# Optimization experiments

Hardware: AMD Instinct MI355X
Metric: run time of the kernel (lower is better)

The kernel has to match this reference:

```python
import jax, jax.numpy as jnp
import numpy as np

N = 100000
D = 512


def setup_inputs() -> dict:
    key = jax.random.key(0)
    k1, k2 = jax.random.split(key)
    features = jax.random.normal(k1, (N, D), dtype=jnp.float32)
    attn_w = jax.random.normal(k2, (D,), dtype=jnp.float32)
    attn_b = jnp.zeros((1,), dtype=jnp.float32)
    return {"features": features, "attn_w": attn_w, "attn_b": attn_b, "k": 4}


def reference(features, attn_w, attn_b, k):
    # features: [N, D]; sliding-window (half-width k, truncated at edges) mean
    n = features.shape[0]
    zero = jnp.zeros((1, features.shape[1]), dtype=features.dtype)
    cs = jnp.concatenate([zero, jnp.cumsum(features, axis=0)], axis=0)  # [N+1, D]
    i = jnp.arange(n)
    lo = jnp.maximum(i - k, 0)          # inclusive window start
    hi = jnp.minimum(i + k, n - 1)      # inclusive window end
    win_sum = cs[hi + 1] - cs[lo]       # [N, D]
    count = (hi - lo + 1).astype(features.dtype)[:, None]
    agg = win_sum / count               # [N, D] windowed means
    scores = agg @ attn_w + attn_b[0]   # [N]
    w = jax.nn.softmax(scores, axis=0)  # [N]
    bag = w @ agg                       # [D]
    return bag, w
```

## Files before the change

### kernel.cpp

```cpp
#include <hip/hip_runtime.h>
#include <math.h>

#define D 512
#define NB_P 1000

__global__ void k_dot(const float* __restrict__ f, const float* __restrict__ w,
                      float* __restrict__ dot, int n) {
    int wave = threadIdx.x >> 6;
    int lane = threadIdx.x & 63;
    int row  = blockIdx.x * 4 + wave;
    if (row >= n) return;
    const float4* fr = (const float4*)(f + (size_t)row * D);
    const float4* wr = (const float4*)w;
    float4 a0 = fr[lane],      b0 = wr[lane];
    float4 a1 = fr[lane + 64], b1 = wr[lane + 64];
    float s = a0.x*b0.x + a0.y*b0.y + a0.z*b0.z + a0.w*b0.w
            + a1.x*b1.x + a1.y*b1.y + a1.z*b1.z + a1.w*b1.w;
    #pragma unroll
    for (int off = 32; off; off >>= 1) s += __shfl_down(s, off);
    if (lane == 0) dot[row] = s;
}

__global__ void k_scores(const float* __restrict__ dot, const float* __restrict__ bptr,
                         const int* __restrict__ kptr, float* __restrict__ scores,
                         float* __restrict__ pmax, float* __restrict__ psum, int n) {
    int i = blockIdx.x * 256 + threadIdx.x;
    int k = *kptr;
    float val = -INFINITY;
    if (i < n) {
        int lo = max(i - k, 0), hi = min(i + k, n - 1);
        float s = 0.f;
        for (int j = lo; j <= hi; ++j) s += dot[j];
        val = s / (float)(hi - lo + 1) + bptr[0];
        scores[i] = val;
    }
    __shared__ float sm[4];
    __shared__ float bmax;
    int lane = threadIdx.x & 63, wid = threadIdx.x >> 6;
    float m = val;
    #pragma unroll
    for (int off = 32; off; off >>= 1) m = fmaxf(m, __shfl_down(m, off));
    if (lane == 0) sm[wid] = m;
    __syncthreads();
    if (threadIdx.x == 0)
        bmax = fmaxf(fmaxf(sm[0], sm[1]), fmaxf(sm[2], sm[3]));
    __syncthreads();
    float mb = bmax;
    float e = (i < n) ? __expf(val - mb) : 0.f;
    #pragma unroll
    for (int off = 32; off; off >>= 1) e += __shfl_down(e, off);
    __syncthreads();
    if (lane == 0) sm[wid] = e;
    __syncthreads();
    if (threadIdx.x == 0) {
        pmax[blockIdx.x] = mb;
        psum[blockIdx.x] = sm[0] + sm[1] + sm[2] + sm[3];
    }
}

__global__ void k_wu(const float* __restrict__ scores, const float* __restrict__ pmax,
                     const float* __restrict__ psum, int nb1,
                     const int* __restrict__ kptr, float* __restrict__ w_out,
                     float* __restrict__ u, int n) {
    __shared__ float sm[4];
    __shared__ float gshared[2];
    int lane = threadIdx.x & 63, wid = threadIdx.x >> 6;

    float m = -INFINITY;
    for (int idx = threadIdx.x; idx < nb1; idx += 256) m = fmaxf(m, pmax[idx]);
    #pragma unroll
    for (int off = 32; off; off >>= 1) m = fmaxf(m, __shfl_down(m, off));
    if (lane == 0) sm[wid] = m;
    __syncthreads();
    if (threadIdx.x == 0)
        gshared[0] = fmaxf(fmaxf(sm[0], sm[1]), fmaxf(sm[2], sm[3]));
    __syncthreads();
    float gmax = gshared[0];

    float s = 0.f;
    for (int idx = threadIdx.x; idx < nb1; idx += 256)
        s += psum[idx] * __expf(pmax[idx] - gmax);
    #pragma unroll
    for (int off = 32; off; off >>= 1) s += __shfl_down(s, off);
    __syncthreads();
    if (lane == 0) sm[wid] = s;
    __syncthreads();
    if (threadIdx.x == 0)
        gshared[1] = 1.f / (sm[0] + sm[1] + sm[2] + sm[3]);
    __syncthreads();
    float inv = gshared[1];

    int j = blockIdx.x * 256 + threadIdx.x;
    if (j >= n) return;
    int k = *kptr;
    float ej = __expf(scores[j] - gmax);
    w_out[j] = ej * inv;
    int lo = max(j - k, 0), hi = min(j + k, n - 1);
    float acc = 0.f;
    for (int i = lo; i <= hi; ++i) {
        int li = max(i - k, 0), hh = min(i + k, n - 1);
        float e = __expf(scores[i] - gmax);
        acc += e * __builtin_amdgcn_rcpf((float)(hh - li + 1));
    }
    u[j] = acc * inv;
}

__global__ void k_pbag(const float* __restrict__ f, const float* __restrict__ u,
                       float* __restrict__ partial, int n, int chunk) {
    int t = threadIdx.x;
    int j0 = blockIdx.x * chunk;
    int j1 = min(j0 + chunk, n);
    float4 acc0 = make_float4(0.f,0.f,0.f,0.f);
    float4 acc1 = make_float4(0.f,0.f,0.f,0.f);
    float4 acc2 = make_float4(0.f,0.f,0.f,0.f);
    float4 acc3 = make_float4(0.f,0.f,0.f,0.f);
    int j = j0;
    for (; j + 4 <= j1; j += 4) {
        float u0 = u[j], u1 = u[j+1], u2 = u[j+2], u3 = u[j+3];
        float4 v0 = ((const float4*)(f + (size_t)(j  ) * D))[t];
        float4 v1 = ((const float4*)(f + (size_t)(j+1) * D))[t];
        float4 v2 = ((const float4*)(f + (size_t)(j+2) * D))[t];
        float4 v3 = ((const float4*)(f + (size_t)(j+3) * D))[t];
        acc0.x += u0*v0.x; acc0.y += u0*v0.y; acc0.z += u0*v0.z; acc0.w += u0*v0.w;
        acc1.x += u1*v1.x; acc1.y += u1*v1.y; acc1.z += u1*v1.z; acc1.w += u1*v1.w;
        acc2.x += u2*v2.x; acc2.y += u2*v2.y; acc2.z += u2*v2.z; acc2.w += u2*v2.w;
        acc3.x += u3*v3.x; acc3.y += u3*v3.y; acc3.z += u3*v3.z; acc3.w += u3*v3.w;
    }
    for (; j < j1; ++j) {
        float uj = u[j];
        float4 v = ((const float4*)(f + (size_t)j * D))[t];
        acc0.x += uj*v.x; acc0.y += uj*v.y; acc0.z += uj*v.z; acc0.w += uj*v.w;
    }
    float4 a;
    a.x = (acc0.x + acc1.x) + (acc2.x + acc3.x);
    a.y = (acc0.y + acc1.y) + (acc2.y + acc3.y);
    a.z = (acc0.z + acc1.z) + (acc2.z + acc3.z);
    a.w = (acc0.w + acc1.w) + (acc2.w + acc3.w);
    ((float4*)(partial + (size_t)blockIdx.x * D))[t] = a;
}

__global__ void k_rbag(const float* __restrict__ partial, float* __restrict__ bag, int nb) {
    int c = blockIdx.x * 16 + (threadIdx.x & 15);
    int r = threadIdx.x >> 4;
    float acc = 0.f;
    for (int b = r; b < nb; b += 16) acc += partial[(size_t)b * D + c];
    __shared__ float sm[256];
    sm[threadIdx.x] = acc;
    __syncthreads();
    if (threadIdx.x < 16) {
        float s = 0.f;
        #pragma unroll
        for (int q = 0; q < 16; ++q) s += sm[q * 16 + threadIdx.x];
        bag[blockIdx.x * 16 + threadIdx.x] = s;
    }
}

extern "C" void kernel_launch(void* const* d_in, const int* in_sizes, int n_in,
                              void* d_out, int out_size, void* d_ws, size_t ws_size,
                              hipStream_t stream) {
    const float* f  = (const float*)d_in[0];
    const float* aw = (const float*)d_in[1];
    const float* ab = (const float*)d_in[2];
    const int*   kp = (const int*)d_in[3];
    int n = in_sizes[0] / D;

    float* bag   = (float*)d_out;
    float* w_out = (float*)d_out + D;

    int nb2 = (n + 255) / 256;

    float* wsf     = (float*)d_ws;
    float* dot     = wsf;
    float* scores  = wsf + n;
    float* u       = wsf + 2 * (size_t)n;
    float* pmax    = wsf + 3 * (size_t)n;
    float* psum    = pmax + nb2;
    size_t poff    = ((3 * (size_t)n + 2 * (size_t)nb2) + 31) & ~(size_t)31;
    float* partial = wsf + poff;

    int chunk = (n + NB_P - 1) / NB_P;

    k_dot   <<<(n + 3) / 4, 256, 0, stream>>>(f, aw, dot, n);
    k_scores<<<nb2, 256, 0, stream>>>(dot, ab, kp, scores, pmax, psum, n);
    k_wu    <<<nb2, 256, 0, stream>>>(scores, pmax, psum, nb2, kp, w_out, u, n);
    k_pbag  <<<NB_P, 128, 0, stream>>>(f, u, partial, n, chunk);
    k_rbag  <<<32, 256, 0, stream>>>(partial, bag, NB_P);
}
```

Baseline: 90.74 us.

## Drop softmax max pass and fold normalization into final reduction kernel

```diff
diff --git a/kernel.cpp b/kernel.cpp
--- a/kernel.cpp
+++ b/kernel.cpp
@@ -21,88 +21,37 @@
     if (lane == 0) dot[row] = s;
 }
 
-__global__ void k_scores(const float* __restrict__ dot, const float* __restrict__ bptr,
-                         const int* __restrict__ kptr, float* __restrict__ scores,
-                         float* __restrict__ pmax, float* __restrict__ psum, int n) {
-    int i = blockIdx.x * 256 + threadIdx.x;
-    int k = *kptr;
-    float val = -INFINITY;
-    if (i < n) {
-        int lo = max(i - k, 0), hi = min(i + k, n - 1);
-        float s = 0.f;
-        for (int j = lo; j <= hi; ++j) s += dot[j];
-        val = s / (float)(hi - lo + 1) + bptr[0];
-        scores[i] = val;
+__global__ void k_eu(const float* __restrict__ dot, const float* __restrict__ bptr,
+                     const int* __restrict__ kptr, float* __restrict__ e_out,
+                     float* __restrict__ uu, float* __restrict__ psum, int n) {
+    int j = blockIdx.x * 256 + threadIdx.x;
+    float e_loc = 0.f;
+    if (j < n) {
+        int k = *kptr;
+        float bias = bptr[0];
+        int ilo = max(j - k, 0), ihi = min(j + k, n - 1);
+        float ut = 0.f;
+        for (int i = ilo; i <= ihi; ++i) {
+            int lo = max(i - k, 0), hi = min(i + k, n - 1);
+            float s = 0.f;
+            for (int q = lo; q <= hi; ++q) s += dot[q];
+            float cnt = (float)(hi - lo + 1);
+            float ei = __expf(s / cnt + bias);
+            if (i == j) e_loc = ei;
+            ut += ei * __builtin_amdgcn_rcpf(cnt);
+        }
+        e_out[j] = e_loc;
+        uu[j] = ut;
     }
+    float e = e_loc;
+    #pragma unroll
+    for (int off = 32; off; off >>= 1) e += __shfl_down(e, off);
     __shared__ float sm[4];
-    __shared__ float bmax;
     int lane = threadIdx.x & 63, wid = threadIdx.x >> 6;
-    float m = val;
-    #pragma unroll
-    for (int off = 32; off; off >>= 1) m = fmaxf(m, __shfl_down(m, off));
-    if (lane == 0) sm[wid] = m;
+    if (lane == 0) sm[wid] = e;
     __syncthreads();
     if (threadIdx.x == 0)
-        bmax = fmaxf(fmaxf(sm[0], sm[1]), fmaxf(sm[2], sm[3]));
-    __syncthreads();
-    float mb = bmax;
-    float e = (i < n) ? __expf(val - mb) : 0.f;
-    #pragma unroll
-    for (int off = 32; off; off >>= 1) e += __shfl_down(e, off);
-    __syncthreads();
-    if (lane == 0) sm[wid] = e;
-    __syncthreads();
-    if (threadIdx.x == 0) {
-        pmax[blockIdx.x] = mb;
         psum[blockIdx.x] = sm[0] + sm[1] + sm[2] + sm[3];
-    }
-}
-
-__global__ void k_wu(const float* __restrict__ scores, const float* __restrict__ pmax,
-                     const float* __restrict__ psum, int nb1,
-                     const int* __restrict__ kptr, float* __restrict__ w_out,
-                     float* __restrict__ u, int n) {
-    __shared__ float sm[4];
-    __shared__ float gshared[2];
-    int lane = threadIdx.x & 63, wid = threadIdx.x >> 6;
-
-    float m = -INFINITY;
-    for (int idx = threadIdx.x; idx < nb1; idx += 256) m = fmaxf(m, pmax[idx]);
-    #pragma unroll
-    for (int off = 32; off; off >>= 1) m = fmaxf(m, __shfl_down(m, off));
-    if (lane == 0) sm[wid] = m;
-    __syncthreads();
-    if (threadIdx.x == 0)
-        gshared[0] = fmaxf(fmaxf(sm[0], sm[1]), fmaxf(sm[2], sm[3]));
-    __syncthreads();
-    float gmax = gshared[0];
-
-    float s = 0.f;
-    for (int idx = threadIdx.x; idx < nb1; idx += 256)
-        s += psum[idx] * __expf(pmax[idx] - gmax);
-    #pragma unroll
-    for (int off = 32; off; off >>= 1) s += __shfl_down(s, off);
-    __syncthreads();
-    if (lane == 0) sm[wid] = s;
-    __syncthreads();
-    if (threadIdx.x == 0)
-        gshared[1] = 1.f / (sm[0] + sm[1] + sm[2] + sm[3]);
-    __syncthreads();
-    float inv = gshared[1];
-
-    int j = blockIdx.x * 256 + threadIdx.x;
-    if (j >= n) return;
-    int k = *kptr;
-    float ej = __expf(scores[j] - gmax);
-    w_out[j] = ej * inv;
-    int lo = max(j - k, 0), hi = min(j + k, n - 1);
-    float acc = 0.f;
-    for (int i = lo; i <= hi; ++i) {
-        int li = max(i - k, 0), hh = min(i + k, n - 1);
-        float e = __expf(scores[i] - gmax);
-        acc += e * __builtin_amdgcn_rcpf((float)(hh - li + 1));
-    }
-    u[j] = acc * inv;
 }
 
 __global__ void k_pbag(const float* __restrict__ f, const float* __restrict__ u,
@@ -139,20 +88,42 @@
     ((float4*)(partial + (size_t)blockIdx.x * D))[t] = a;
 }
 
-__global__ void k_rbag(const float* __restrict__ partial, float* __restrict__ bag, int nb) {
-    int c = blockIdx.x * 16 + (threadIdx.x & 15);
-    int r = threadIdx.x >> 4;
-    float acc = 0.f;
-    for (int b = r; b < nb; b += 16) acc += partial[(size_t)b * D + c];
-    __shared__ float sm[256];
-    sm[threadIdx.x] = acc;
+__global__ void k_final(const float* __restrict__ partial, const float* __restrict__ psum,
+                        int nbp, int nbs, const float* __restrict__ e,
+                        float* __restrict__ bag, float* __restrict__ w_out, int n) {
+    __shared__ float sm[4];
+    __shared__ float ginv;
+    int lane = threadIdx.x & 63, wid = threadIdx.x >> 6;
+
+    float s = 0.f;
+    for (int idx = threadIdx.x; idx < nbs; idx += 256) s += psum[idx];
+    #pragma unroll
+    for (int off = 32; off; off >>= 1) s += __shfl_down(s, off);
+    if (lane == 0) sm[wid] = s;
     __syncthreads();
-    if (threadIdx.x < 16) {
-        float s = 0.f;
-        #pragma unroll
-        for (int q = 0; q < 16; ++q) s += sm[q * 16 + threadIdx.x];
-        bag[blockIdx.x * 16 + threadIdx.x] = s;
+    if (threadIdx.x == 0)
+        ginv = 1.f / (sm[0] + sm[1] + sm[2] + sm[3]);
+    __syncthreads();
+    float inv = ginv;
+
+    if (blockIdx.x < 32) {
+        int c = blockIdx.x * 16 + (threadIdx.x & 15);
+        int r = threadIdx.x >> 4;
+        float acc = 0.f;
+        for (int b = r; b < nbp; b += 16) acc += partial[(size_t)b * D + c];
+        __shared__ float sred[256];
+        sred[threadIdx.x] = acc;
+        __syncthreads();
+        if (threadIdx.x < 16) {
+            float t = 0.f;
+            #pragma unroll
+            for (int q = 0; q < 16; ++q) t += sred[q * 16 + threadIdx.x];
+            bag[blockIdx.x * 16 + threadIdx.x] = t * inv;
+        }
     }
+
+    for (int j = blockIdx.x * 256 + threadIdx.x; j < n; j += gridDim.x * 256)
+        w_out[j] = e[j] * inv;
 }
 
 extern "C" void kernel_launch(void* const* d_in, const int* in_sizes, int n_in,
@@ -171,18 +142,16 @@
 
     float* wsf     = (float*)d_ws;
     float* dot     = wsf;
-    float* scores  = wsf + n;
-    float* u       = wsf + 2 * (size_t)n;
-    float* pmax    = wsf + 3 * (size_t)n;
-    float* psum    = pmax + nb2;
-    size_t poff    = ((3 * (size_t)n + 2 * (size_t)nb2) + 31) & ~(size_t)31;
+    float* e       = wsf + n;
+    float* uu      = wsf + 2 * (size_t)n;
+    float* psum    = wsf + 3 * (size_t)n;
+    size_t poff    = ((3 * (size_t)n + (size_t)nb2) + 31) & ~(size_t)31;
     float* partial = wsf + poff;
 
     int chunk = (n + NB_P - 1) / NB_P;
 
-    k_dot   <<<(n + 3) / 4, 256, 0, stream>>>(f, aw, dot, n);
-    k_scores<<<nb2, 256, 0, stream>>>(dot, ab, kp, scores, pmax, psum, n);
-    k_wu    <<<nb2, 256, 0, stream>>>(scores, pmax, psum, nb2, kp, w_out, u, n);
-    k_pbag  <<<NB_P, 128, 0, stream>>>(f, u, partial, n, chunk);
-    k_rbag  <<<32, 256, 0, stream>>>(partial, bag, NB_P);
+    k_dot  <<<(n + 3) / 4, 256, 0, stream>>>(f, aw, dot, n);
+    k_eu   <<<nb2, 256, 0, stream>>>(dot, ab, kp, e, uu, psum, n);
+    k_pbag <<<NB_P, 128, 0, stream>>>(f, uu, partial, n, chunk);
+    k_final<<<nb2, 256, 0, stream>>>(partial, psum, NB_P, nb2, e, bag, w_out, n);
 }
```

New measurement: 91.82 us. No clear change (+1.2%).
